# Kernel tuning notes

Hardware: AMD Instinct MI355X
Metric: run time of the kernel (lower is better)

The kernel has to match this reference:

```python
import jax, jax.numpy as jnp
import numpy as np

B, T, D = 2, 2048, 1024
H, DH, P = 16, 64, 512


def setup_inputs() -> dict:
    key = jax.random.key(0)
    ks = jax.random.split(key, 7)
    s = 0.02
    return {
        "x": jax.random.normal(ks[0], (B, T, D), jnp.float32),
        "prefix_k": jax.random.normal(ks[1], (B, H, P, DH), jnp.float32),
        "prefix_v": jax.random.normal(ks[2], (B, H, P, DH), jnp.float32),
        "Wq": jax.random.normal(ks[3], (D, D), jnp.float32) * s,
        "Wk": jax.random.normal(ks[4], (D, D), jnp.float32) * s,
        "Wv": jax.random.normal(ks[5], (D, D), jnp.float32) * s,
        "Wo": jax.random.normal(ks[6], (D, D), jnp.float32) * s,
    }


def reference(x, prefix_k, prefix_v, Wq, Wk, Wv, Wo):
    b, t, c = x.shape
    h, dh = H, DH
    # nn.Linear without bias: y = x @ W.T
    q = (x @ Wq.T).reshape(b, t, h, dh).transpose(0, 2, 1, 3)  # [B,H,T,Dh]
    k = (x @ Wk.T).reshape(b, t, h, dh).transpose(0, 2, 1, 3)
    v = (x @ Wv.T).reshape(b, t, h, dh).transpose(0, 2, 1, 3)
    k = jnp.concatenate([prefix_k, k], axis=2)  # [B,H,P+T,Dh]
    v = jnp.concatenate([prefix_v, v], axis=2)
    scale = 1.0 / jnp.sqrt(jnp.float32(dh))
    att = jnp.einsum("bhqd,bhkd->bhqk", q, k) * scale  # [B,H,T,P+T]
    att = jax.nn.softmax(att, axis=-1)  # no causal mask in source
    y = jnp.einsum("bhqk,bhkd->bhqd", att, v)  # [B,H,T,Dh]
    y = y.transpose(0, 2, 1, 3).reshape(b, t, c)
    return y @ Wo.T
```

## Files before the change

kernel.cpp:

```cpp
#include <hip/hip_runtime.h>
#include <cstdint>

#define Bv  2
#define Tv  2048
#define Dv  1024
#define Hv  16
#define DHv 64
#define Pv  512
#define Lv  2560
#define NT  (Lv / 64)

typedef __attribute__((ext_vector_type(8))) short sh8;
typedef __attribute__((ext_vector_type(4))) short sh4;
typedef __attribute__((ext_vector_type(4))) float f4;
typedef __attribute__((ext_vector_type(4))) unsigned int u4v;

#define MFMA(a,b,c) __builtin_amdgcn_mfma_f32_16x16x32_bf16(a,b,c,0,0,0)

__device__ __forceinline__ unsigned short bf16_rn(float f) {
    unsigned int u = __builtin_bit_cast(unsigned int, f);
    u += 0x7FFFu + ((u >> 16) & 1u);
    return (unsigned short)(u >> 16);
}
__device__ __forceinline__ float bf16_f(unsigned short h) {
    unsigned int u = ((unsigned int)h) << 16;
    return __builtin_bit_cast(float, u);
}
__device__ __forceinline__ unsigned int fbits(float f) {
    return __builtin_bit_cast(unsigned int, f);
}

__device__ __forceinline__ void gload16(const unsigned short* g, unsigned short* l) {
    __builtin_amdgcn_global_load_lds(
        (const __attribute__((address_space(1))) unsigned int*)(g),
        (__attribute__((address_space(3))) unsigned int*)(l),
        16, 0, 0);
}

__device__ __forceinline__ sh8 packP(const f4 a, const f4 b) {
    float e0 = __builtin_amdgcn_exp2f(a[0]), e1 = __builtin_amdgcn_exp2f(a[1]);
    float e2 = __builtin_amdgcn_exp2f(a[2]), e3 = __builtin_amdgcn_exp2f(a[3]);
    float f0 = __builtin_amdgcn_exp2f(b[0]), f1 = __builtin_amdgcn_exp2f(b[1]);
    float f2 = __builtin_amdgcn_exp2f(b[2]), f3 = __builtin_amdgcn_exp2f(b[3]);
    u4v d;
    d[0] = __builtin_amdgcn_perm(fbits(e1), fbits(e0), 0x07060302u);
    d[1] = __builtin_amdgcn_perm(fbits(e3), fbits(e2), 0x07060302u);
    d[2] = __builtin_amdgcn_perm(fbits(f1), fbits(f0), 0x07060302u);
    d[3] = __builtin_amdgcn_perm(fbits(f3), fbits(f2), 0x07060302u);
    return __builtin_bit_cast(sh8, d);
}

__global__ __launch_bounds__(256) void prep_all(
    const float* __restrict__ x,  const float* __restrict__ Wq,
    const float* __restrict__ Wk, const float* __restrict__ Wv,
    const float* __restrict__ pk, const float* __restrict__ Wo,
    const float* __restrict__ pv,
    unsigned short* __restrict__ xb,  unsigned short* __restrict__ wqb,
    unsigned short* __restrict__ wkb, unsigned short* __restrict__ wvb,
    unsigned short* __restrict__ pkb, unsigned short* __restrict__ woh,
    unsigned short* __restrict__ pvtb)
{
    __shared__ unsigned short Tls[64][66];
    const int blk = blockIdx.x;
    const int tid = threadIdx.x;
    if (blk < 9216) {
        int i = blk * 256 + tid;
        const float* src; unsigned short* dst; int off;
        if      (i < 1048576) { src = x;  dst = xb;  off = i; }
        else if (i < 1310720) { src = Wq; dst = wqb; off = i - 1048576; }
        else if (i < 1572864) { src = Wk; dst = wkb; off = i - 1310720; }
        else if (i < 1835008) { src = Wv; dst = wvb; off = i - 1572864; }
        else if (i < 2097152) { src = pk; dst = pkb; off = i - 1835008; }
        else                  { src = Wo; dst = woh; off = i - 2097152; }
        float4 v = reinterpret_cast<const float4*>(src)[off];
        sh4 h;
        h[0] = (short)bf16_rn(v.x); h[1] = (short)bf16_rn(v.y);
        h[2] = (short)bf16_rn(v.z); h[3] = (short)bf16_rn(v.w);
        reinterpret_cast<sh4*>(dst)[off] = h;
    } else {
        const int bb = blk - 9216;
        const int bh = bb >> 3, pt = bb & 7;
        #pragma unroll
        for (int i = 0; i < 4; i++) {
            int id = i * 256 + tid;
            int p = id >> 4, c4 = (id & 15) << 2;
            float4 v = *reinterpret_cast<const float4*>(
                &pv[((size_t)bh * Pv + pt * 64 + p) * DHv + c4]);
            Tls[c4+0][p] = bf16_rn(v.x);
            Tls[c4+1][p] = bf16_rn(v.y);
            Tls[c4+2][p] = bf16_rn(v.z);
            Tls[c4+3][p] = bf16_rn(v.w);
        }
        __syncthreads();
        #pragma unroll
        for (int i = 0; i < 2; i++) {
            int id = i * 256 + tid;
            int d = id >> 3, u = id & 7;
            sh4 lo, hi;
            #pragma unroll
            for (int j = 0; j < 4; j++) {
                lo[j] = (short)Tls[d][u * 8 + j];
                hi[j] = (short)Tls[d][u * 8 + 4 + j];
            }
            int p0 = ((u >> 2) & 1) * 32 + (u & 1) * 16 + ((u >> 1) & 1) * 4;
            size_t base = ((size_t)bh * DHv + d) * Pv + pt * 64;
            *reinterpret_cast<sh4*>(&pvtb[base + p0])     = lo;
            *reinterpret_cast<sh4*>(&pvtb[base + p0 + 8]) = hi;
        }
    }
}

__global__ __launch_bounds__(256) void qkv_gemm(
    const unsigned short* __restrict__ xb,
    const unsigned short* __restrict__ wqb, const unsigned short* __restrict__ wkb,
    const unsigned short* __restrict__ wvb,
    unsigned short* __restrict__ qb, unsigned short* __restrict__ kb,
    unsigned short* __restrict__ vtb)
{
    __shared__ __align__(16) unsigned short As[128 * 64], Bs[128 * 64];
    const int tid = threadIdx.x;
    const int lane = tid & 63, w = tid >> 6;
    const int g = lane >> 4, tx = lane & 15;
    const int wr = w >> 1, wc = w & 1;
    const int m0 = blockIdx.x * 128, n0 = blockIdx.y * 128;
    const int z = blockIdx.z;
    const unsigned short* Wb = (z == 0) ? wqb : (z == 1) ? wkb : wvb;
    const int srow = lane >> 3, scol = lane & 7;

    f4 acc[4][4] = {};

    for (int k0 = 0; k0 < Dv; k0 += 64) {
        #pragma unroll
        for (int c = 0; c < 4; c++) {
            int row = w * 32 + c * 8 + srow;
            int su = (scol ^ (row & 7)) << 3;
            gload16(&xb[(size_t)(m0 + row) * Dv + k0 + su], &As[(w * 32 + c * 8) * 64]);
            gload16(&Wb[(size_t)(n0 + row) * Dv + k0 + su], &Bs[(w * 32 + c * 8) * 64]);
        }
        __syncthreads();
        #pragma unroll
        for (int ks = 0; ks < 2; ks++) {
            sh8 fa[4], fb[4];
            #pragma unroll
            for (int mi = 0; mi < 4; mi++) {
                int r = wr * 64 + mi * 16 + tx;
                fa[mi] = *reinterpret_cast<const sh8*>(&As[(r * 64 + ks * 32 + g * 8) ^ ((r & 7) << 3)]);
            }
            #pragma unroll
            for (int ni = 0; ni < 4; ni++) {
                int r = wc * 64 + ni * 16 + tx;
                fb[ni] = *reinterpret_cast<const sh8*>(&Bs[(r * 64 + ks * 32 + g * 8) ^ ((r & 7) << 3)]);
            }
            if (z < 2) {
                #pragma unroll
                for (int mi = 0; mi < 4; mi++)
                    #pragma unroll
                    for (int ni = 0; ni < 4; ni++)
                        acc[mi][ni] = MFMA(fb[ni], fa[mi], acc[mi][ni]);
            } else {
                #pragma unroll
                for (int mi = 0; mi < 4; mi++)
                    #pragma unroll
                    for (int ni = 0; ni < 4; ni++)
                        acc[mi][ni] = MFMA(fa[mi], fb[ni], acc[mi][ni]);
            }
        }
        __syncthreads();
    }

    if (z < 2) {
        unsigned short* ob = (z == 0) ? qb : kb;
        const float sc = (z == 0) ? 0.1803368801f : 1.0f;
        #pragma unroll
        for (int mi = 0; mi < 4; mi++)
            #pragma unroll
            for (int ni = 0; ni < 4; ni++) {
                int m = m0 + wr * 64 + mi * 16 + tx;
                int n = n0 + wc * 64 + ni * 16 + g * 4;
                sh4 pkd;
                #pragma unroll
                for (int i = 0; i < 4; i++) pkd[i] = (short)bf16_rn(acc[mi][ni][i] * sc);
                *reinterpret_cast<sh4*>(&ob[(size_t)m * Dv + n]) = pkd;
            }
    } else {
        const int tb0 = ((m0 + wr * 64) & (Tv - 1));
        const int b   = (m0 + wr * 64) >> 11;
        #pragma unroll
        for (int mi = 0; mi < 4; mi++)
            #pragma unroll
            for (int ni = 0; ni < 4; ni++) {
                int t = tb0 + ((mi & 2) << 4) + (g << 3) + ((mi & 1) << 2);
                int n = n0 + wc * 64 + ni * 16 + tx;
                int h = n >> 6, dh = n & 63;
                sh4 pkd;
                #pragma unroll
                for (int i = 0; i < 4; i++) pkd[i] = (short)bf16_rn(acc[mi][ni][i]);
                *reinterpret_cast<sh4*>(&vtb[(((size_t)(b * Hv + h)) * DHv + dh) * Tv + t]) = pkd;
            }
    }
}

__global__ __launch_bounds__(256) void flash_mfma(
    const unsigned short* __restrict__ qbuf, const unsigned short* __restrict__ kb,
    const unsigned short* __restrict__ vtb,
    const unsigned short* __restrict__ pkb, const unsigned short* __restrict__ pvtb,
    unsigned short* __restrict__ yh)
{
    __shared__ __align__(16) unsigned short Ks[3][64 * 64], Vs[3][64 * 64];
    __shared__ float olex[2][4][64];
    const int tid = threadIdx.x;
    const int lane = tid & 63, w = tid >> 6;
    const int kw = w & 1, qw = w >> 1;
    const int g = lane >> 4, tx = lane & 15;
    const int pblk = blockIdx.x;
    const int L = (pblk & 7) * 64 + (pblk >> 3);
    const int qt = L & 15;
    const int bh = L >> 4;
    const int b = bh >> 4, h = bh & 15;
    const int srow = lane >> 3, scol = lane & 7;

    sh8 qf[4][2];
    #pragma unroll
    for (int qg = 0; qg < 4; qg++) {
        size_t base = ((size_t)(b * Tv) + qt * 128 + qw * 64 + qg * 16 + tx) * Dv + h * 64;
        qf[qg][0] = *reinterpret_cast<const sh8*>(&qbuf[base + g * 8]);
        qf[qg][1] = *reinterpret_cast<const sh8*>(&qbuf[base + 32 + g * 8]);
    }

    f4 o[4][4] = {};
    f4 ol[4] = {};
    sh8 onesf;
    #pragma unroll
    for (int j = 0; j < 8; j++) onesf[j] = (short)0x3F80;

    const int r0 = w * 16 + srow, r1 = r0 + 8;
    const int su0 = (scol ^ (r0 & 7)) << 3;
    const int su1 = (scol ^ (r1 & 7)) << 3;
    const unsigned short* ka0 = &pkb[((size_t)bh * Pv + r0) * DHv + su0];
    const unsigned short* ka1 = &pkb[((size_t)bh * Pv + r1) * DHv + su1];
    const unsigned short* va0 = &pvtb[((size_t)bh * DHv + r0) * Pv + su0];
    const unsigned short* va1 = &pvtb[((size_t)bh * DHv + r1) * Pv + su1];

    auto stage = [&](int buf) {
        gload16(ka0, &Ks[buf][(w * 16    ) * 64]);
        gload16(ka1, &Ks[buf][(w * 16 + 8) * 64]);
        gload16(va0, &Vs[buf][(w * 16    ) * 64]);
        gload16(va1, &Vs[buf][(w * 16 + 8) * 64]);
    };
    auto advance = [&](int nt) {
        if (nt == 7) {
            ka0 = &kb[((size_t)(b * Tv) + r0) * Dv + h * 64 + su0];
            ka1 = &kb[((size_t)(b * Tv) + r1) * Dv + h * 64 + su1];
            va0 = &vtb[((size_t)bh * DHv + r0) * Tv + su0];
            va1 = &vtb[((size_t)bh * DHv + r1) * Tv + su1];
        } else if (nt < 7) { ka0 += 64 * DHv; ka1 += 64 * DHv; va0 += 64; va1 += 64; }
        else               { ka0 += 64 * Dv;  ka1 += 64 * Dv;  va0 += 64; va1 += 64; }
    };

    auto compute = [&](int cur) {
        sh8 kf[2][2], vf[4];
        #pragma unroll
        for (int nf = 0; nf < 2; nf++) {
            int rk = 32 * kw + nf * 16 + tx;
            kf[nf][0] = *reinterpret_cast<const sh8*>(
                &Ks[cur][(rk * 64 + g * 8) ^ ((rk & 7) << 3)]);
            kf[nf][1] = *reinterpret_cast<const sh8*>(
                &Ks[cur][(rk * 64 + 32 + g * 8) ^ ((rk & 7) << 3)]);
        }
        #pragma unroll
        for (int nf = 0; nf < 4; nf++) {
            int rv = nf * 16 + tx;
            vf[nf] = *reinterpret_cast<const sh8*>(
                &Vs[cur][(rv * 64 + 32 * kw + g * 8) ^ ((rv & 7) << 3)]);
        }
        #pragma unroll
        for (int qg = 0; qg < 4; qg++) {
            f4 sa = {}, sb = {};
            sa = MFMA(kf[0][0], qf[qg][0], sa); sa = MFMA(kf[0][1], qf[qg][1], sa);
            sb = MFMA(kf[1][0], qf[qg][0], sb); sb = MFMA(kf[1][1], qf[qg][1], sb);
            sh8 pf = packP(sa, sb);
            #pragma unroll
            for (int nf = 0; nf < 4; nf++)
                o[qg][nf] = MFMA(vf[nf], pf, o[qg][nf]);
            ol[qg] = MFMA(onesf, pf, ol[qg]);
        }
    };

    stage(0); advance(0);
    stage(1); advance(1);
    int cur = 0, stg = 2;

    #pragma unroll 1
    for (int t = 0; t < NT - 2; t++) {
        asm volatile("s_waitcnt vmcnt(4)" ::: "memory");
        __builtin_amdgcn_s_barrier();
        __builtin_amdgcn_sched_barrier(0);
        stage(stg); advance(t + 2);
        compute(cur);
        __builtin_amdgcn_sched_barrier(0);
        cur = (cur == 2) ? 0 : cur + 1;
        stg = (stg == 2) ? 0 : stg + 1;
    }
    asm volatile("s_waitcnt vmcnt(4)" ::: "memory");
    __builtin_amdgcn_s_barrier();
    __builtin_amdgcn_sched_barrier(0);
    compute(cur);
    __builtin_amdgcn_sched_barrier(0);
    cur = (cur == 2) ? 0 : cur + 1;
    asm volatile("s_waitcnt vmcnt(0)" ::: "memory");
    __builtin_amdgcn_s_barrier();
    __builtin_amdgcn_sched_barrier(0);
    compute(cur);

    float* ex = qw ? reinterpret_cast<float*>(Vs) : reinterpret_cast<float*>(Ks);
    if (kw) {
        #pragma unroll
        for (int qg = 0; qg < 4; qg++) {
            #pragma unroll
            for (int nf = 0; nf < 4; nf++)
                *reinterpret_cast<f4*>(&ex[((qg * 4 + nf) * 64 + lane) * 4]) = o[qg][nf];
            olex[qw][qg][lane] = ol[qg][0];
        }
    }
    __syncthreads();
    if (!kw) {
        #pragma unroll
        for (int qg = 0; qg < 4; qg++) {
            float l = ol[qg][0] + olex[qw][qg][lane];
            float inv = 1.0f / l;
            size_t ybase = ((size_t)(b * Tv) + qt * 128 + qw * 64 + qg * 16 + tx) * Dv + h * 64;
            #pragma unroll
            for (int nf = 0; nf < 4; nf++) {
                f4 op = o[qg][nf] +
                    *reinterpret_cast<const f4*>(&ex[((qg * 4 + nf) * 64 + lane) * 4]);
                sh4 ph;
                #pragma unroll
                for (int i = 0; i < 4; i++) ph[i] = (short)bf16_rn(op[i] * inv);
                *reinterpret_cast<sh4*>(&yh[ybase + nf * 16 + g * 4]) = ph;
            }
        }
    }
}

__global__ __launch_bounds__(256) void out_gemm(
    const unsigned short* __restrict__ yh,
    const unsigned short* __restrict__ woh,
    float* __restrict__ out)
{
    __shared__ __align__(16) unsigned short As[64 * 64], Bs[128 * 64];
    const int tid = threadIdx.x;
    const int lane = tid & 63, w = tid >> 6;
    const int g = lane >> 4, tx = lane & 15;
    const int wr = w >> 1, wc = w & 1;
    const int m0 = blockIdx.x * 64, n0 = blockIdx.y * 128;
    const int srow = lane >> 3, scol = lane & 7;

    f4 acc[2][4] = {};

    for (int k0 = 0; k0 < Dv; k0 += 64) {
        #pragma unroll
        for (int c = 0; c < 2; c++) {
            int row = w * 16 + c * 8 + srow;
            int su = (scol ^ (row & 7)) << 3;
            gload16(&yh[(size_t)(m0 + row) * Dv + k0 + su], &As[(w * 16 + c * 8) * 64]);
        }
        #pragma unroll
        for (int c = 0; c < 4; c++) {
            int row = w * 32 + c * 8 + srow;
            int su = (scol ^ (row & 7)) << 3;
            gload16(&woh[(size_t)(n0 + row) * Dv + k0 + su], &Bs[(w * 32 + c * 8) * 64]);
        }
        __syncthreads();
        #pragma unroll
        for (int ks = 0; ks < 2; ks++) {
            sh8 fa[2], fb[4];
            #pragma unroll
            for (int mi = 0; mi < 2; mi++) {
                int r = wr * 32 + mi * 16 + tx;
                fa[mi] = *reinterpret_cast<const sh8*>(&As[(r * 64 + ks * 32 + g * 8) ^ ((r & 7) << 3)]);
            }
            #pragma unroll
            for (int ni = 0; ni < 4; ni++) {
                int r = wc * 64 + ni * 16 + tx;
                fb[ni] = *reinterpret_cast<const sh8*>(&Bs[(r * 64 + ks * 32 + g * 8) ^ ((r & 7) << 3)]);
            }
            #pragma unroll
            for (int mi = 0; mi < 2; mi++)
                #pragma unroll
                for (int ni = 0; ni < 4; ni++)
                    acc[mi][ni] = MFMA(fb[ni], fa[mi], acc[mi][ni]);
        }
        __syncthreads();
    }

    #pragma unroll
    for (int mi = 0; mi < 2; mi++)
        #pragma unroll
        for (int ni = 0; ni < 4; ni++) {
            int m = m0 + wr * 32 + mi * 16 + tx;
            int n = n0 + wc * 64 + ni * 16 + g * 4;
            *reinterpret_cast<float4*>(&out[(size_t)m * Dv + n]) =
                make_float4(acc[mi][ni][0], acc[mi][ni][1], acc[mi][ni][2], acc[mi][ni][3]);
        }
}

extern "C" void kernel_launch(void* const* d_in, const int* in_sizes, int n_in,
                              void* d_out, int out_size, void* d_ws, size_t ws_size,
                              hipStream_t stream)
{
    const float* x  = (const float*)d_in[0];
    const float* pk = (const float*)d_in[1];
    const float* pv = (const float*)d_in[2];
    const float* Wq = (const float*)d_in[3];
    const float* Wk = (const float*)d_in[4];
    const float* Wv = (const float*)d_in[5];
    const float* Wo = (const float*)d_in[6];

    const size_t M1 = 1048576;
    unsigned short* ws  = (unsigned short*)d_ws;
    unsigned short* xb   = ws;
    unsigned short* wqb  = ws + 4  * M1;
    unsigned short* wkb  = ws + 5  * M1;
    unsigned short* wvb  = ws + 6  * M1;
    unsigned short* woh  = ws + 7  * M1;
    unsigned short* pkb  = ws + 8  * M1;
    unsigned short* pvtb = ws + 9  * M1;
    unsigned short* qb   = ws + 10 * M1;
    unsigned short* kb   = ws + 14 * M1;
    unsigned short* vtb  = ws + 18 * M1;
    unsigned short* yh   = ws + 22 * M1;

    prep_all<<<9472, 256, 0, stream>>>(x, Wq, Wk, Wv, pk, Wo, pv,
                                       xb, wqb, wkb, wvb, pkb, woh, pvtb);
    qkv_gemm<<<dim3(32, 8, 3), 256, 0, stream>>>(xb, wqb, wkb, wvb, qb, kb, vtb);
    flash_mfma<<<dim3(Bv * Hv * (Tv / 128)), 256, 0, stream>>>(qb, kb, vtb, pkb, pvtb, yh);
    out_gemm<<<dim3(64, 8), 256, 0, stream>>>(yh, woh, (float*)d_out);
}
```

Before: 120.9 us.

## Double-buffer LDS tiles in QKV and output GEMMs with async prefetch

Both projection GEMMs now keep two LDS buffers and issue the direct-to-LDS global loads for step t+2 while step t is being computed. Partial vmcnt waits and explicit barriers replace the two full __syncthreads per iteration. The aim is to hide global-load latency behind MFMA work. In exchange, LDS use per block doubles, which may lower occupancy, and correctness depends on the hand-counted vmcnt thresholds.

```diff
diff --git a/kernel.cpp b/kernel.cpp
--- a/kernel.cpp
+++ b/kernel.cpp
@@ -117,7 +117,7 @@
     unsigned short* __restrict__ qb, unsigned short* __restrict__ kb,
     unsigned short* __restrict__ vtb)
 {
-    __shared__ __align__(16) unsigned short As[128 * 64], Bs[128 * 64];
+    __shared__ __align__(16) unsigned short As[2][128 * 64], Bs[2][128 * 64];
     const int tid = threadIdx.x;
     const int lane = tid & 63, w = tid >> 6;
     const int g = lane >> 4, tx = lane & 15;
@@ -129,27 +129,31 @@
 
     f4 acc[4][4] = {};
 
-    for (int k0 = 0; k0 < Dv; k0 += 64) {
+    auto stage = [&](int buf, int step) {
+        int k0 = step * 64;
         #pragma unroll
         for (int c = 0; c < 4; c++) {
             int row = w * 32 + c * 8 + srow;
             int su = (scol ^ (row & 7)) << 3;
-            gload16(&xb[(size_t)(m0 + row) * Dv + k0 + su], &As[(w * 32 + c * 8) * 64]);
-            gload16(&Wb[(size_t)(n0 + row) * Dv + k0 + su], &Bs[(w * 32 + c * 8) * 64]);
-        }
-        __syncthreads();
+            gload16(&xb[(size_t)(m0 + row) * Dv + k0 + su], &As[buf][(w * 32 + c * 8) * 64]);
+            gload16(&Wb[(size_t)(n0 + row) * Dv + k0 + su], &Bs[buf][(w * 32 + c * 8) * 64]);
+        }
+    };
+    auto compute = [&](int buf) {
         #pragma unroll
         for (int ks = 0; ks < 2; ks++) {
             sh8 fa[4], fb[4];
             #pragma unroll
             for (int mi = 0; mi < 4; mi++) {
                 int r = wr * 64 + mi * 16 + tx;
-                fa[mi] = *reinterpret_cast<const sh8*>(&As[(r * 64 + ks * 32 + g * 8) ^ ((r & 7) << 3)]);
+                fa[mi] = *reinterpret_cast<const sh8*>(
+                    &As[buf][(r * 64 + ks * 32 + g * 8) ^ ((r & 7) << 3)]);
             }
             #pragma unroll
             for (int ni = 0; ni < 4; ni++) {
                 int r = wc * 64 + ni * 16 + tx;
-                fb[ni] = *reinterpret_cast<const sh8*>(&Bs[(r * 64 + ks * 32 + g * 8) ^ ((r & 7) << 3)]);
+                fb[ni] = *reinterpret_cast<const sh8*>(
+                    &Bs[buf][(r * 64 + ks * 32 + g * 8) ^ ((r & 7) << 3)]);
             }
             if (z < 2) {
                 #pragma unroll
@@ -165,7 +169,20 @@
                         acc[mi][ni] = MFMA(fa[mi], fb[ni], acc[mi][ni]);
             }
         }
-        __syncthreads();
+    };
+
+    stage(0, 0); stage(1, 1);
+    #pragma unroll 1
+    for (int t = 0; t < 16; t++) {
+        const int cur = t & 1;
+        if (t < 15) asm volatile("s_waitcnt vmcnt(8)" ::: "memory");
+        else        asm volatile("s_waitcnt vmcnt(0)" ::: "memory");
+        __builtin_amdgcn_s_barrier();
+        __builtin_amdgcn_sched_barrier(0);
+        compute(cur);
+        __builtin_amdgcn_sched_barrier(0);
+        __builtin_amdgcn_s_barrier();
+        if (t + 2 < 16) stage(cur, t + 2);
     }
 
     if (z < 2) {
@@ -347,7 +364,7 @@
     const unsigned short* __restrict__ woh,
     float* __restrict__ out)
 {
-    __shared__ __align__(16) unsigned short As[64 * 64], Bs[128 * 64];
+    __shared__ __align__(16) unsigned short As[2][64 * 64], Bs[2][128 * 64];
     const int tid = threadIdx.x;
     const int lane = tid & 63, w = tid >> 6;
     const int g = lane >> 4, tx = lane & 15;
@@ -357,32 +374,36 @@
 
     f4 acc[2][4] = {};
 
-    for (int k0 = 0; k0 < Dv; k0 += 64) {
+    auto stage = [&](int buf, int step) {
+        int k0 = step * 64;
         #pragma unroll
         for (int c = 0; c < 2; c++) {
             int row = w * 16 + c * 8 + srow;
             int su = (scol ^ (row & 7)) << 3;
-            gload16(&yh[(size_t)(m0 + row) * Dv + k0 + su], &As[(w * 16 + c * 8) * 64]);
+            gload16(&yh[(size_t)(m0 + row) * Dv + k0 + su], &As[buf][(w * 16 + c * 8) * 64]);
         }
         #pragma unroll
         for (int c = 0; c < 4; c++) {
             int row = w * 32 + c * 8 + srow;
             int su = (scol ^ (row & 7)) << 3;
-            gload16(&woh[(size_t)(n0 + row) * Dv + k0 + su], &Bs[(w * 32 + c * 8) * 64]);
-        }
-        __syncthreads();
+            gload16(&woh[(size_t)(n0 + row) * Dv + k0 + su], &Bs[buf][(w * 32 + c * 8) * 64]);
+        }
+    };
+    auto compute = [&](int buf) {
         #pragma unroll
         for (int ks = 0; ks < 2; ks++) {
             sh8 fa[2], fb[4];
             #pragma unroll
             for (int mi = 0; mi < 2; mi++) {
                 int r = wr * 32 + mi * 16 + tx;
-                fa[mi] = *reinterpret_cast<const sh8*>(&As[(r * 64 + ks * 32 + g * 8) ^ ((r & 7) << 3)]);
+                fa[mi] = *reinterpret_cast<const sh8*>(
+                    &As[buf][(r * 64 + ks * 32 + g * 8) ^ ((r & 7) << 3)]);
             }
             #pragma unroll
             for (int ni = 0; ni < 4; ni++) {
                 int r = wc * 64 + ni * 16 + tx;
-                fb[ni] = *reinterpret_cast<const sh8*>(&Bs[(r * 64 + ks * 32 + g * 8) ^ ((r & 7) << 3)]);
+                fb[ni] = *reinterpret_cast<const sh8*>(
+                    &Bs[buf][(r * 64 + ks * 32 + g * 8) ^ ((r & 7) << 3)]);
             }
             #pragma unroll
             for (int mi = 0; mi < 2; mi++)
@@ -390,7 +411,20 @@
                 for (int ni = 0; ni < 4; ni++)
                     acc[mi][ni] = MFMA(fb[ni], fa[mi], acc[mi][ni]);
         }
-        __syncthreads();
+    };
+
+    stage(0, 0); stage(1, 1);
+    #pragma unroll 1
+    for (int t = 0; t < 16; t++) {
+        const int cur = t & 1;
+        if (t < 15) asm volatile("s_waitcnt vmcnt(6)" ::: "memory");
+        else        asm volatile("s_waitcnt vmcnt(0)" ::: "memory");
+        __builtin_amdgcn_s_barrier();
+        __builtin_amdgcn_sched_barrier(0);
+        compute(cur);
+        __builtin_amdgcn_sched_barrier(0);
+        __builtin_amdgcn_s_barrier();
+        if (t + 2 < 16) stage(cur, t + 2);
     }
 
     #pragma unroll
```

Result: no change. 120.6 us, median of 2 (-0.2%).
